# Performance work log

Hardware: AMD Instinct MI355X
Metric: run time of the kernel (lower is better)

Reference implementation:

```python
import jax, jax.numpy as jnp
import numpy as np

N = 4096   # nodes
E = 65536  # edges
D_IN = 64
H = 128
T = 8
B = 8


def setup_inputs() -> dict:
    key = jax.random.key(0)
    ks = jax.random.split(key, 6)
    x = jax.random.normal(ks[0], (B, T, N, D_IN), jnp.float32)
    edge_index = jax.random.randint(ks[1], (2, E), 0, N, dtype=jnp.int32)
    W0 = jax.random.normal(ks[2], (D_IN + H, 4 * H), jnp.float32) * 0.05
    b0 = jax.random.normal(ks[3], (4 * H,), jnp.float32) * 0.05
    W1 = jax.random.normal(ks[4], (H + H, 4 * H), jnp.float32) * 0.05
    b1 = jax.random.normal(ks[5], (4 * H,), jnp.float32) * 0.05
    return {"x": x, "W0": W0, "b0": b0, "W1": W1, "b1": b1, "edge_index": edge_index}


def _gcn_norm(edge_index, n):
    # PyG GCNConv(improved=True): A_hat = A + 2I, deg over incoming edges (col)
    src, dst = edge_index[0], edge_index[1]
    deg = jax.ops.segment_sum(jnp.ones(edge_index.shape[1], jnp.float32), dst, num_segments=n) + 2.0
    dinv = jax.lax.rsqrt(deg)  # deg >= 2 always, safe
    return src, dst, dinv


def _gcn_gates(comb, W, b, src, dst, dinv, n):
    # comb: (b, n, i+h) -> gates: (b, n, 4h)
    xw = jnp.einsum('bnf,fg->bng', comb, W)
    norm_e = dinv[src] * dinv[dst]                      # (E,)
    msgs = xw[:, src, :] * norm_e[None, :, None]        # (b, E, 4h)
    agg = jax.vmap(lambda m: jax.ops.segment_sum(m, dst, num_segments=n))(msgs)
    # self-loop with weight 2: norm = 2 * dinv[i]^2
    agg = agg + (2.0 * dinv * dinv)[None, :, None] * xw + b
    return agg


def reference(x, W0, b0, W1, b1, edge_index):
    src, dst, dinv = _gcn_norm(edge_index, N)

    def run_layer(seq, W, b):
        h_dim = W.shape[1] // 4

        def step(carry, xt):
            h, c = carry
            comb = jnp.concatenate([xt, h], axis=-1)
            gates = _gcn_gates(comb, W, b, src, dst, dinv, N)
            ci, cf, co, cg = jnp.split(gates, 4, axis=-1)
            i = jax.nn.sigmoid(ci)
            f = jax.nn.sigmoid(cf)
            o = jax.nn.sigmoid(co)
            g = jnp.tanh(cg)
            c_next = f * c + i * g
            h_next = o * jnp.tanh(c_next)
            return (h_next, c_next), h_next

        h0 = jnp.zeros((seq.shape[1], N, h_dim), seq.dtype)
        _, hs = jax.lax.scan(step, (h0, h0), seq)
        return hs  # (t, b, n, h)

    seq = jnp.swapaxes(x, 0, 1)  # batch_first -> (t, b, n, d)
    hs0 = run_layer(seq, W0, b0)
    hs1 = run_layer(hs0, W1, b1)
    return jnp.swapaxes(hs1, 0, 1)  # (b, t, n, h) last-layer output sequence
```

## Files before the change

kernel.cpp:

```cpp
#include <hip/hip_runtime.h>
#include <hip/hip_fp16.h>
#include <math.h>

constexpr int N_NODES = 4096;
constexpr int N_EDGES = 65536;
constexpr int D_INF   = 64;
constexpr int H       = 128;
constexpr int T       = 8;
constexpr int B       = 8;
constexpr int M       = B * N_NODES;

typedef __attribute__((ext_vector_type(8))) short bf16x8;
typedef __attribute__((ext_vector_type(4))) float f32x4;
typedef __attribute__((ext_vector_type(8))) _Float16 f16x8;

__device__ inline unsigned short f2bf(float x) {
  unsigned int u = __float_as_uint(x);
  unsigned int r = (u + 0x7fffu + ((u >> 16) & 1u)) >> 16;
  return (unsigned short)r;
}
__device__ inline float bf2f(unsigned short b) {
  return __uint_as_float((unsigned int)b << 16);
}
__device__ __forceinline__ int swz(int s) { return s ^ (((s >> 7) & 7) << 3); }


__global__ void k_count(const int* __restrict__ dst, int* __restrict__ cnt) {
  int e = blockIdx.x * blockDim.x + threadIdx.x;
  if (e < N_EDGES) atomicAdd(&cnt[dst[e]], 1);
}

__global__ void k_dinv(const int* __restrict__ cnt, float* __restrict__ dinv) {
  int n = blockIdx.x * blockDim.x + threadIdx.x;
  if (n < N_NODES) dinv[n] = 1.0f / sqrtf((float)cnt[n] + 2.0f);
}

__global__ void k_scan(const int* __restrict__ cnt, int* __restrict__ rowptr) {
  __shared__ int sums[1024];
  int t = threadIdx.x;
  int v0 = cnt[4*t+0], v1 = cnt[4*t+1], v2 = cnt[4*t+2], v3 = cnt[4*t+3];
  int s0 = v0, s1 = s0 + v1, s2 = s1 + v2, s3 = s2 + v3;
  sums[t] = s3;
  __syncthreads();
  for (int off = 1; off < 1024; off <<= 1) {
    int x = (t >= off) ? sums[t - off] : 0;
    __syncthreads();
    sums[t] += x;
    __syncthreads();
  }
  int base = (t > 0) ? sums[t - 1] : 0;
  if (t == 0) rowptr[0] = 0;
  rowptr[4*t+1] = base + s0;
  rowptr[4*t+2] = base + s1;
  rowptr[4*t+3] = base + s2;
  rowptr[4*t+4] = base + s3;
}

__global__ void k_fill(const int* __restrict__ src, const int* __restrict__ dst,
                       const float* __restrict__ dinv, const int* __restrict__ rowptr,
                       int* __restrict__ fill, int2* __restrict__ eg) {
  int e = blockIdx.x * blockDim.x + threadIdx.x;
  if (e >= N_EDGES) return;
  int s = src[e], d = dst[e];
  int p = rowptr[d] + atomicAdd(&fill[d], 1);
  eg[p] = make_int2(s, __float_as_int(dinv[s] * dinv[d]));
}

__global__ void k_hist(const int* __restrict__ cnt, int* __restrict__ hist) {
  int n = blockIdx.x * blockDim.x + threadIdx.x;
  if (n < N_NODES) atomicAdd(&hist[min(cnt[n], 127)], 1);
}

__global__ void k_hscan(const int* __restrict__ hist, int* __restrict__ hbase) {
  __shared__ int sh[128];
  int t = threadIdx.x;
  sh[t] = hist[t];
  __syncthreads();
  for (int off = 1; off < 128; off <<= 1) {
    int x = (t >= off) ? sh[t - off] : 0;
    __syncthreads();
    sh[t] += x;
    __syncthreads();
  }
  hbase[t] = sh[t] - hist[t];
}

__global__ void k_place(const int* __restrict__ cnt, const int* __restrict__ hbase,
                        int* __restrict__ filld, int* __restrict__ sorted) {
  int n = blockIdx.x * blockDim.x + threadIdx.x;
  if (n >= N_NODES) return;
  int d = min(cnt[n], 127);
  sorted[hbase[d] + atomicAdd(&filld[d], 1)] = n;
}

__global__ void k_pack(const float* __restrict__ W, unsigned short* __restrict__ Bp,
                       int K) {
  int tid = blockIdx.x * 256 + threadIdx.x;
  if (tid >= K * 64) return;
  int lane = tid & 63;
  int ntg  = (tid >> 6) & 31;
  int kb   = tid >> 11;
  int gate = ntg & 3, fg = ntg >> 2;
  int corig = gate * 128 + fg * 16 + (lane & 15);
  int k0 = kb * 32 + (lane >> 4) * 8;
  long obase = ((long)(kb * 32 + ntg) * 64 + lane) * 8;
  long plane = (long)K * 512;
  #pragma unroll
  for (int j = 0; j < 8; ++j) {
    float v = W[(long)(k0 + j) * 512 + corig];
    unsigned short h = f2bf(v);
    Bp[obase + j]         = h;
    Bp[plane + obase + j] = f2bf(v - bf2f(h));
  }
}

template<int K, bool L0>
__global__ __launch_bounds__(512, 4) void k_fused(
    const int* __restrict__ rowptr, const int2* __restrict__ eg,
    const float* __restrict__ dinv, const int* __restrict__ sorted,
    const float* __restrict__ X32,
    const _Float16* __restrict__ PH0,
    const _Float16* __restrict__ PH1,
    const unsigned short* __restrict__ Bp, const float* __restrict__ bias,
    _Float16* __restrict__ hout, float* __restrict__ cbuf,
    float* __restrict__ out2, int t) {
  constexpr int KB = K / 32;
  __shared__ __align__(16) unsigned short At[8 * KB * 64 * 8];
  __shared__ int nodeLDS[64];
  int tid  = threadIdx.x;
  int lane = tid & 63;
  int w    = tid >> 6;
  int j    = blockIdx.x;
  int b    = j & 7;
  int jj   = j >> 3;
  int g    = lane >> 4, l = lane & 15;
  int c4   = l * 4, c8 = l * 8;

  const float*    Ax   = L0 ? (X32 + (long)b * ((long)T * N_NODES * D_INF)) : nullptr;
  const _Float16* Ah_p = L0 ? nullptr : (PH0 + (long)b * N_NODES * H);
  const _Float16* Bh_p = (L0 ? PH0 : PH1) + (long)b * N_NODES * H;
  constexpr int kbB0 = (L0 ? 64 : 128) >> 5;
  int lane2f = 16 * (l & 3);
  int kbB    = kbB0 + (c8 >> 5);
  int kbA16  = c8 >> 5;
  int kbA32  = c4 >> 5;
  int subA32 = (l & 7) >> 1;
  int j0A32  = (l & 1) * 4;

  #pragma unroll
  for (int nd = 0; nd < 2; ++nd) {
    int r  = (w << 3) + (g << 1) + nd;
    int pairIdx = jj * 32 + (r >> 1);
    int n  = (r & 1) ? sorted[N_NODES - 1 - pairIdx] : sorted[pairIdx];
    if (l == 0) nodeLDS[r] = n;
    int rs = rowptr[n], re = rowptr[n + 1];
    float accA[8] = {0.f,0.f,0.f,0.f,0.f,0.f,0.f,0.f};
    float accB[8] = {0.f,0.f,0.f,0.f,0.f,0.f,0.f,0.f};
    int e = rs;
    for (; e + 3 < re; e += 4) {
      int2 q0 = eg[e], q1 = eg[e + 1], q2 = eg[e + 2], q3 = eg[e + 3];
      float w0 = __int_as_float(q0.y), w1 = __int_as_float(q1.y);
      float w2 = __int_as_float(q2.y), w3 = __int_as_float(q3.y);
      if constexpr (L0) {
        f32x4 a0 = *(const f32x4*)(Ax + (long)q0.x * D_INF + c4);
        f32x4 a1 = *(const f32x4*)(Ax + (long)q1.x * D_INF + c4);
        f32x4 a2 = *(const f32x4*)(Ax + (long)q2.x * D_INF + c4);
        f32x4 a3 = *(const f32x4*)(Ax + (long)q3.x * D_INF + c4);
        #pragma unroll
        for (int q = 0; q < 4; ++q)
          accA[q] += w0 * a0[q] + w1 * a1[q] + w2 * a2[q] + w3 * a3[q];
      } else {
        f16x8 a0 = *(const f16x8*)(Ah_p + (long)q0.x * H + c8);
        f16x8 a1 = *(const f16x8*)(Ah_p + (long)q1.x * H + c8);
        f16x8 a2 = *(const f16x8*)(Ah_p + (long)q2.x * H + c8);
        f16x8 a3 = *(const f16x8*)(Ah_p + (long)q3.x * H + c8);
        #pragma unroll
        for (int q = 0; q < 8; ++q)
          accA[q] += w0 * (float)a0[q] + w1 * (float)a1[q]
                   + w2 * (float)a2[q] + w3 * (float)a3[q];
      }
      f16x8 b0 = *(const f16x8*)(Bh_p + (long)q0.x * H + c8);
      f16x8 b1 = *(const f16x8*)(Bh_p + (long)q1.x * H + c8);
      f16x8 b2 = *(const f16x8*)(Bh_p + (long)q2.x * H + c8);
      f16x8 b3 = *(const f16x8*)(Bh_p + (long)q3.x * H + c8);
      #pragma unroll
      for (int q = 0; q < 8; ++q)
        accB[q] += w0 * (float)b0[q] + w1 * (float)b1[q]
                 + w2 * (float)b2[q] + w3 * (float)b3[q];
    }
    for (; e < re; ++e) {
      int2 q0 = eg[e];
      float w0 = __int_as_float(q0.y);
      if constexpr (L0) {
        f32x4 a0 = *(const f32x4*)(Ax + (long)q0.x * D_INF + c4);
        #pragma unroll
        for (int q = 0; q < 4; ++q) accA[q] += w0 * a0[q];
      } else {
        f16x8 a0 = *(const f16x8*)(Ah_p + (long)q0.x * H + c8);
        #pragma unroll
        for (int q = 0; q < 8; ++q) accA[q] += w0 * (float)a0[q];
      }
      f16x8 b0 = *(const f16x8*)(Bh_p + (long)q0.x * H + c8);
      #pragma unroll
      for (int q = 0; q < 8; ++q) accB[q] += w0 * (float)b0[q];
    }
    float dn = dinv[n];
    float sw = 2.0f * dn * dn;
    if constexpr (L0) {
      f32x4 a = *(const f32x4*)(Ax + (long)n * D_INF + c4);
      #pragma unroll
      for (int q = 0; q < 4; ++q) accA[q] += sw * a[q];
    } else {
      f16x8 a = *(const f16x8*)(Ah_p + (long)n * H + c8);
      #pragma unroll
      for (int q = 0; q < 8; ++q) accA[q] += sw * (float)a[q];
    }
    {
      f16x8 v = *(const f16x8*)(Bh_p + (long)n * H + c8);
      #pragma unroll
      for (int q = 0; q < 8; ++q) accB[q] += sw * (float)v[q];
    }

    int mt    = r >> 4;
    int lane2 = (r & 15) + lane2f;
    {
      bf16x8 hv, lv;
      #pragma unroll
      for (int q = 0; q < 8; ++q) {
        unsigned short hs = f2bf(accB[q]);
        hv[q] = (short)hs;
        lv[q] = (short)f2bf(accB[q] - bf2f(hs));
      }
      *(bf16x8*)(At + swz((((mt)     * KB + kbB) * 64 + lane2) * 8)) = hv;
      *(bf16x8*)(At + swz((((4 + mt) * KB + kbB) * 64 + lane2) * 8)) = lv;
    }
    if constexpr (L0) {
      unsigned long long hv = 0ull, lv = 0ull;
      #pragma unroll
      for (int q = 0; q < 4; ++q) {
        unsigned short hs = f2bf(accA[q]);
        unsigned short ls = f2bf(accA[q] - bf2f(hs));
        hv |= (unsigned long long)hs << (16 * q);
        lv |= (unsigned long long)ls << (16 * q);
      }
      int lA = (r & 15) + 16 * subA32;
      *(unsigned long long*)(At + swz((((mt)     * KB + kbA32) * 64 + lA) * 8 + j0A32)) = hv;
      *(unsigned long long*)(At + swz((((4 + mt) * KB + kbA32) * 64 + lA) * 8 + j0A32)) = lv;
    } else {
      bf16x8 hv, lv;
      #pragma unroll
      for (int q = 0; q < 8; ++q) {
        unsigned short hs = f2bf(accA[q]);
        hv[q] = (short)hs;
        lv[q] = (short)f2bf(accA[q] - bf2f(hs));
      }
      *(bf16x8*)(At + swz((((mt)     * KB + kbA16) * 64 + lane2) * 8)) = hv;
      *(bf16x8*)(At + swz((((4 + mt) * KB + kbA16) * 64 + lane2) * 8)) = lv;
    }
  }
  __syncthreads();

  int l15 = lane & 15, lq = lane >> 4;
  const unsigned short* bb  = Bp + (long)(w * 4) * 512 + lane * 8;
  const unsigned short* blp = bb + (long)K * 512;

  f32x4 acc[4][4];
  #pragma unroll
  for (int mt = 0; mt < 4; ++mt)
    #pragma unroll
    for (int gt = 0; gt < 4; ++gt)
      acc[mt][gt] = (f32x4){0.f, 0.f, 0.f, 0.f};

  __builtin_amdgcn_s_setprio(1);
  #pragma unroll 2
  for (int kb = 0; kb < KB; ++kb) {
    bf16x8 AH_[4], AL_[4];
    #pragma unroll
    for (int mt = 0; mt < 4; ++mt) {
      AH_[mt] = *(const bf16x8*)(At + swz((((mt)     * KB + kb) * 64 + lane) * 8));
      AL_[mt] = *(const bf16x8*)(At + swz((((4 + mt) * KB + kb) * 64 + lane) * 8));
    }
    bf16x8 BH[4], BL[4];
    #pragma unroll
    for (int gt = 0; gt < 4; ++gt) {
      BH[gt] = *(const bf16x8*)(bb  + ((long)kb * 32 + gt) * 512);
      BL[gt] = *(const bf16x8*)(blp + ((long)kb * 32 + gt) * 512);
    }
    #pragma unroll
    for (int gt = 0; gt < 4; ++gt) {
      #pragma unroll
      for (int mt = 0; mt < 4; ++mt) {
        acc[mt][gt] = __builtin_amdgcn_mfma_f32_16x16x32_bf16(AH_[mt], BH[gt], acc[mt][gt], 0, 0, 0);
        acc[mt][gt] = __builtin_amdgcn_mfma_f32_16x16x32_bf16(AL_[mt], BH[gt], acc[mt][gt], 0, 0, 0);
        acc[mt][gt] = __builtin_amdgcn_mfma_f32_16x16x32_bf16(AH_[mt], BL[gt], acc[mt][gt], 0, 0, 0);
      }
    }
  }
  __builtin_amdgcn_s_setprio(0);

  int f = w * 16 + l15;
  float bi = bias[f], bff = bias[128 + f], bo = bias[256 + f], bg = bias[384 + f];
  #pragma unroll
  for (int mt = 0; mt < 4; ++mt) {
    #pragma unroll
    for (int r = 0; r < 4; ++r) {
      int rt = mt * 16 + lq * 4 + r;
      int n2 = nodeLDS[rt];
      float vi = 1.0f / (1.0f + __expf(-(acc[mt][0][r] + bi)));
      float vf = 1.0f / (1.0f + __expf(-(acc[mt][1][r] + bff)));
      float vo = 1.0f / (1.0f + __expf(-(acc[mt][2][r] + bo)));
      float vg = tanhf(acc[mt][3][r] + bg);
      long idx = ((long)b * N_NODES + n2) * H + f;
      float cn = vf * cbuf[idx] + vi * vg;
      float hn = vo * tanhf(cn);
      cbuf[idx] = cn;
      hout[idx] = (_Float16)hn;
      if (out2) {
        __builtin_nontemporal_store(hn,
            &out2[(((long)b * T + t) * N_NODES + n2) * H + f]);
      }
    }
  }
}


extern "C" void kernel_launch(void* const* d_in, const int* in_sizes, int n_in,
                              void* d_out, int out_size, void* d_ws, size_t ws_size,
                              hipStream_t stream) {
  const float* x  = (const float*)d_in[0];
  const float* W0 = (const float*)d_in[1];
  const float* b0 = (const float*)d_in[2];
  const float* W1 = (const float*)d_in[3];
  const float* b1 = (const float*)d_in[4];
  const int*   ei = (const int*)d_in[5];
  const int* srcp = ei;
  const int* dstp = ei + N_EDGES;
  float* out = (float*)d_out;

  char* p = (char*)d_ws;
  auto alloc = [&](size_t bytes) {
    char* r = p;
    p += (bytes + 255) & ~(size_t)255;
    return r;
  };
  int*   cnt    = (int*)  alloc(N_NODES * 4);
  int*   fill   = (int*)  alloc(N_NODES * 4);
  float* dinv   = (float*)alloc(N_NODES * 4);
  int*   rowptr = (int*)  alloc((N_NODES + 1) * 4);
  int2*  eg     = (int2*) alloc((size_t)N_EDGES * 8);
  int*   hist   = (int*)  alloc(128 * 4);
  int*   hbase  = (int*)  alloc(128 * 4);
  int*   filld  = (int*)  alloc(128 * 4);
  int*   sorted = (int*)  alloc(N_NODES * 4);
  float* cc     = (float*)alloc((size_t)2 * M * H * 4);
  _Float16* hh  = (_Float16*)alloc((size_t)4 * M * H * 2);
  unsigned short* Bp0 = (unsigned short*)alloc((size_t)192 * 512 * 2 * 2);
  unsigned short* Bp1 = (unsigned short*)alloc((size_t)256 * 512 * 2 * 2);
  float*    c0  = cc;
  float*    c1  = cc + (size_t)M * H;
  _Float16* h0a = hh;
  _Float16* h0b = hh + (size_t)M * H;
  _Float16* h1a = hh + (size_t)2 * M * H;
  _Float16* h1b = hh + (size_t)3 * M * H;

  hipMemsetAsync(cnt,   0, N_NODES * 4, stream);
  hipMemsetAsync(fill,  0, N_NODES * 4, stream);
  hipMemsetAsync(hist,  0, 128 * 4, stream);
  hipMemsetAsync(filld, 0, 128 * 4, stream);
  hipMemsetAsync(cc,    0, (size_t)2 * M * H * 4, stream);
  hipMemsetAsync(hh,    0, (size_t)4 * M * H * 2, stream);

  k_count<<<N_EDGES / 256, 256, 0, stream>>>(dstp, cnt);
  k_dinv <<<N_NODES / 256, 256, 0, stream>>>(cnt, dinv);
  k_scan <<<1, 1024, 0, stream>>>(cnt, rowptr);
  k_fill <<<N_EDGES / 256, 256, 0, stream>>>(srcp, dstp, dinv, rowptr, fill, eg);
  k_hist <<<N_NODES / 256, 256, 0, stream>>>(cnt, hist);
  k_hscan<<<1, 128, 0, stream>>>(hist, hbase);
  k_place<<<N_NODES / 256, 256, 0, stream>>>(cnt, hbase, filld, sorted);
  k_pack <<<(192 * 64 + 255) / 256, 256, 0, stream>>>(W0, Bp0, 192);
  k_pack <<<(256 * 64 + 255) / 256, 256, 0, stream>>>(W1, Bp1, 256);

  for (int t = 0; t < T; ++t) {
    const _Float16* h0r = (t & 1) ? h0b : h0a;
    _Float16*       h0w = (t & 1) ? h0a : h0b;
    const _Float16* h1r = (t & 1) ? h1b : h1a;
    _Float16*       h1w = (t & 1) ? h1a : h1b;
    k_fused<192, true><<<512, 512, 0, stream>>>(rowptr, eg, dinv, sorted,
        x + (size_t)t * N_NODES * D_INF, h0r, nullptr,
        Bp0, b0, h0w, c0, nullptr, t);
    k_fused<256, false><<<512, 512, 0, stream>>>(rowptr, eg, dinv, sorted,
        nullptr, h0w, h1r,
        Bp1, b1, h1w, c1, out, t);
  }
}
```

Measured before the change: 772.4 us.

## Reuse layer-1 aggregated h0 for next-step layer-0 and precompute A·x

Layer 1 at step t already computes the graph aggregation A·h0_t. It now also stores that result, already split into hi/lo bf16 in MFMA tile layout, into a global buffer. Layer 0 at step t+1 reads this buffer directly instead of re-gathering h0 over the edges. The A·x aggregation for every timestep is hoisted into one upfront batched kernel and stored as fp16. As a result, layer 0 becomes a pure GEMM plus LSTM-cell kernel. The cost is extra global traffic for the stored tiles and a small precision loss from keeping A·x in fp16.

Measured after the change: 829.5 us. 1.07x slower.

```diff
diff --git a/kernel.cpp b/kernel.cpp
--- a/kernel.cpp
+++ b/kernel.cpp
@@ -13,6 +13,7 @@
 typedef __attribute__((ext_vector_type(8))) short bf16x8;
 typedef __attribute__((ext_vector_type(4))) float f32x4;
 typedef __attribute__((ext_vector_type(8))) _Float16 f16x8;
+typedef __attribute__((ext_vector_type(4))) _Float16 f16x4;
 
 __device__ inline unsigned short f2bf(float x) {
   unsigned int u = __float_as_uint(x);
@@ -114,17 +115,171 @@
   }
 }
 
-template<int K, bool L0>
-__global__ __launch_bounds__(512, 4) void k_fused(
+__global__ __launch_bounds__(256) void k_ax(
+    const int* __restrict__ rowptr, const int2* __restrict__ eg,
+    const float* __restrict__ dinv, const float* __restrict__ x,
+    _Float16* __restrict__ AX) {
+  int tid = threadIdx.x;
+  int grp = blockIdx.x * 16 + (tid >> 4);
+  int l   = tid & 15;
+  int c4  = l * 4;
+  int n   = grp & (N_NODES - 1);
+  int bt  = grp >> 12;
+  int b   = bt & 7, tt = bt >> 3;
+  const float* Xb = x + (long)(b * T + tt) * N_NODES * D_INF;
+  float acc[4] = {0.f, 0.f, 0.f, 0.f};
+  int rs = rowptr[n], re = rowptr[n + 1];
+  int e = rs;
+  for (; e + 3 < re; e += 4) {
+    int2 q0 = eg[e], q1 = eg[e + 1], q2 = eg[e + 2], q3 = eg[e + 3];
+    float w0 = __int_as_float(q0.y), w1 = __int_as_float(q1.y);
+    float w2 = __int_as_float(q2.y), w3 = __int_as_float(q3.y);
+    f32x4 a0 = *(const f32x4*)(Xb + (long)q0.x * D_INF + c4);
+    f32x4 a1 = *(const f32x4*)(Xb + (long)q1.x * D_INF + c4);
+    f32x4 a2 = *(const f32x4*)(Xb + (long)q2.x * D_INF + c4);
+    f32x4 a3 = *(const f32x4*)(Xb + (long)q3.x * D_INF + c4);
+    #pragma unroll
+    for (int q = 0; q < 4; ++q)
+      acc[q] += w0 * a0[q] + w1 * a1[q] + w2 * a2[q] + w3 * a3[q];
+  }
+  for (; e < re; ++e) {
+    int2 q0 = eg[e];
+    float w0 = __int_as_float(q0.y);
+    f32x4 a0 = *(const f32x4*)(Xb + (long)q0.x * D_INF + c4);
+    #pragma unroll
+    for (int q = 0; q < 4; ++q) acc[q] += w0 * a0[q];
+  }
+  float dn = dinv[n];
+  float sw = 2.0f * dn * dn;
+  f32x4 a = *(const f32x4*)(Xb + (long)n * D_INF + c4);
+  #pragma unroll
+  for (int q = 0; q < 4; ++q) acc[q] += sw * a[q];
+  f16x4 o;
+  #pragma unroll
+  for (int q = 0; q < 4; ++q) o[q] = (_Float16)acc[q];
+  *(f16x4*)(AX + ((long)(tt * 8 + b) * N_NODES + n) * D_INF + c4) = o;
+}
+
+__global__ __launch_bounds__(512, 4) void k_l0(
+    const int* __restrict__ sorted,
+    const _Float16* __restrict__ AXt,
+    const unsigned short* __restrict__ AH0,
+    const unsigned short* __restrict__ Bp, const float* __restrict__ bias,
+    _Float16* __restrict__ hout, float* __restrict__ cbuf) {
+  __shared__ __align__(16) unsigned short Atx[8 * 2 * 64 * 8];
+  __shared__ int nodeLDS[64];
+  int tid  = threadIdx.x;
+  int lane = tid & 63;
+  int w    = tid >> 6;
+  int j    = blockIdx.x;
+  int b    = j & 7;
+  int jj   = j >> 3;
+  int g    = lane >> 4, l = lane & 15;
+  int c4   = l * 4;
+  int kbA32  = c4 >> 5;
+  int subA32 = (l & 7) >> 1;
+  int j0A32  = (l & 1) * 4;
+
+  #pragma unroll
+  for (int nd = 0; nd < 2; ++nd) {
+    int r = (w << 3) + (g << 1) + nd;
+    int pairIdx = jj * 32 + (r >> 1);
+    int n = (r & 1) ? sorted[N_NODES - 1 - pairIdx] : sorted[pairIdx];
+    if (l == 0) nodeLDS[r] = n;
+    f16x4 xv = *(const f16x4*)(AXt + ((long)b * N_NODES + n) * D_INF + c4);
+    unsigned long long hv = 0ull, lv = 0ull;
+    #pragma unroll
+    for (int q = 0; q < 4; ++q) {
+      float a = (float)xv[q];
+      unsigned short hs = f2bf(a);
+      unsigned short ls = f2bf(a - bf2f(hs));
+      hv |= (unsigned long long)hs << (16 * q);
+      lv |= (unsigned long long)ls << (16 * q);
+    }
+    int mt = r >> 4;
+    int lA = (r & 15) + 16 * subA32;
+    *(unsigned long long*)(Atx + swz(((mt * 2 + kbA32) * 64 + lA) * 8 + j0A32)) = hv;
+    *(unsigned long long*)(Atx + swz((((4 + mt) * 2 + kbA32) * 64 + lA) * 8 + j0A32)) = lv;
+  }
+  __syncthreads();
+
+  int l15 = lane & 15, lq = lane >> 4;
+  const unsigned short* bb  = Bp + (long)(w * 4) * 512 + lane * 8;
+  const unsigned short* blp = bb + (long)192 * 512;
+
+  f32x4 acc[4][4];
+  #pragma unroll
+  for (int mt = 0; mt < 4; ++mt)
+    #pragma unroll
+    for (int gt = 0; gt < 4; ++gt)
+      acc[mt][gt] = (f32x4){0.f, 0.f, 0.f, 0.f};
+
+  __builtin_amdgcn_s_setprio(1);
+  #pragma unroll
+  for (int kb = 0; kb < 6; ++kb) {
+    bf16x8 AH_[4], AL_[4];
+    if (kb < 2) {
+      #pragma unroll
+      for (int mt = 0; mt < 4; ++mt) {
+        AH_[mt] = *(const bf16x8*)(Atx + swz(((mt * 2 + kb) * 64 + lane) * 8));
+        AL_[mt] = *(const bf16x8*)(Atx + swz((((4 + mt) * 2 + kb) * 64 + lane) * 8));
+      }
+    } else {
+      #pragma unroll
+      for (int mt = 0; mt < 4; ++mt) {
+        AH_[mt] = *(const bf16x8*)(AH0 + ((((long)j * 8 + mt) * 4 + (kb - 2)) * 64 + lane) * 8);
+        AL_[mt] = *(const bf16x8*)(AH0 + ((((long)j * 8 + 4 + mt) * 4 + (kb - 2)) * 64 + lane) * 8);
+      }
+    }
+    bf16x8 BH[4], BL[4];
+    #pragma unroll
+    for (int gt = 0; gt < 4; ++gt) {
+      BH[gt] = *(const bf16x8*)(bb  + ((long)kb * 32 + gt) * 512);
+      BL[gt] = *(const bf16x8*)(blp + ((long)kb * 32 + gt) * 512);
+    }
+    #pragma unroll
+    for (int gt = 0; gt < 4; ++gt) {
+      #pragma unroll
+      for (int mt = 0; mt < 4; ++mt) {
+        acc[mt][gt] = __builtin_amdgcn_mfma_f32_16x16x32_bf16(AH_[mt], BH[gt], acc[mt][gt], 0, 0, 0);
+        acc[mt][gt] = __builtin_amdgcn_mfma_f32_16x16x32_bf16(AL_[mt], BH[gt], acc[mt][gt], 0, 0, 0);
+        acc[mt][gt] = __builtin_amdgcn_mfma_f32_16x16x32_bf16(AH_[mt], BL[gt], acc[mt][gt], 0, 0, 0);
+      }
+    }
+  }
+  __builtin_amdgcn_s_setprio(0);
+
+  int f = w * 16 + l15;
+  float bi = bias[f], bff = bias[128 + f], bo = bias[256 + f], bg = bias[384 + f];
+  #pragma unroll
+  for (int mt = 0; mt < 4; ++mt) {
+    #pragma unroll
+    for (int r = 0; r < 4; ++r) {
+      int rt = mt * 16 + lq * 4 + r;
+      int n2 = nodeLDS[rt];
+      float vi = 1.0f / (1.0f + __expf(-(acc[mt][0][r] + bi)));
+      float vf = 1.0f / (1.0f + __expf(-(acc[mt][1][r] + bff)));
+      float vo = 1.0f / (1.0f + __expf(-(acc[mt][2][r] + bo)));
+      float vg = tanhf(acc[mt][3][r] + bg);
+      long idx = ((long)b * N_NODES + n2) * H + f;
+      float cn = vf * cbuf[idx] + vi * vg;
+      float hn = vo * tanhf(cn);
+      cbuf[idx] = cn;
+      hout[idx] = (_Float16)hn;
+    }
+  }
+}
+
+__global__ __launch_bounds__(512, 4) void k_l1(
     const int* __restrict__ rowptr, const int2* __restrict__ eg,
     const float* __restrict__ dinv, const int* __restrict__ sorted,
-    const float* __restrict__ X32,
-    const _Float16* __restrict__ PH0,
-    const _Float16* __restrict__ PH1,
+    const _Float16* __restrict__ H0,
+    const _Float16* __restrict__ H1r,
     const unsigned short* __restrict__ Bp, const float* __restrict__ bias,
-    _Float16* __restrict__ hout, float* __restrict__ cbuf,
+    unsigned short* __restrict__ AH0,
+    _Float16* __restrict__ h1out, float* __restrict__ cbuf,
     float* __restrict__ out2, int t) {
-  constexpr int KB = K / 32;
+  constexpr int KB = 8;
   __shared__ __align__(16) unsigned short At[8 * KB * 64 * 8];
   __shared__ int nodeLDS[64];
   int tid  = threadIdx.x;
@@ -134,18 +289,12 @@
   int b    = j & 7;
   int jj   = j >> 3;
   int g    = lane >> 4, l = lane & 15;
-  int c4   = l * 4, c8 = l * 8;
-
-  const float*    Ax   = L0 ? (X32 + (long)b * ((long)T * N_NODES * D_INF)) : nullptr;
-  const _Float16* Ah_p = L0 ? nullptr : (PH0 + (long)b * N_NODES * H);
-  const _Float16* Bh_p = (L0 ? PH0 : PH1) + (long)b * N_NODES * H;
-  constexpr int kbB0 = (L0 ? 64 : 128) >> 5;
+  int c8   = l * 8;
+  const _Float16* A_p = H0  + (long)b * N_NODES * H;
+  const _Float16* B_p = H1r + (long)b * N_NODES * H;
   int lane2f = 16 * (l & 3);
-  int kbB    = kbB0 + (c8 >> 5);
   int kbA16  = c8 >> 5;
-  int kbA32  = c4 >> 5;
-  int subA32 = (l & 7) >> 1;
-  int j0A32  = (l & 1) * 4;
+  int kbB    = 4 + kbA16;
 
   #pragma unroll
   for (int nd = 0; nd < 2; ++nd) {
@@ -161,28 +310,18 @@
       int2 q0 = eg[e], q1 = eg[e + 1], q2 = eg[e + 2], q3 = eg[e + 3];
       float w0 = __int_as_float(q0.y), w1 = __int_as_float(q1.y);
       float w2 = __int_as_float(q2.y), w3 = __int_as_float(q3.y);
-      if constexpr (L0) {
-        f32x4 a0 = *(const f32x4*)(Ax + (long)q0.x * D_INF + c4);
-        f32x4 a1 = *(const f32x4*)(Ax + (long)q1.x * D_INF + c4);
-        f32x4 a2 = *(const f32x4*)(Ax + (long)q2.x * D_INF + c4);
-        f32x4 a3 = *(const f32x4*)(Ax + (long)q3.x * D_INF + c4);
-        #pragma unroll
-        for (int q = 0; q < 4; ++q)
-          accA[q] += w0 * a0[q] + w1 * a1[q] + w2 * a2[q] + w3 * a3[q];
-      } else {
-        f16x8 a0 = *(const f16x8*)(Ah_p + (long)q0.x * H + c8);
-        f16x8 a1 = *(const f16x8*)(Ah_p + (long)q1.x * H + c8);
-        f16x8 a2 = *(const f16x8*)(Ah_p + (long)q2.x * H + c8);
-        f16x8 a3 = *(const f16x8*)(Ah_p + (long)q3.x * H + c8);
-        #pragma unroll
-        for (int q = 0; q < 8; ++q)
-          accA[q] += w0 * (float)a0[q] + w1 * (float)a1[q]
-                   + w2 * (float)a2[q] + w3 * (float)a3[q];
-      }
-      f16x8 b0 = *(const f16x8*)(Bh_p + (long)q0.x * H + c8);
-      f16x8 b1 = *(const f16x8*)(Bh_p + (long)q1.x * H + c8);
-      f16x8 b2 = *(const f16x8*)(Bh_p + (long)q2.x * H + c8);
-      f16x8 b3 = *(const f16x8*)(Bh_p + (long)q3.x * H + c8);
+      f16x8 a0 = *(const f16x8*)(A_p + (long)q0.x * H + c8);
+      f16x8 a1 = *(const f16x8*)(A_p + (long)q1.x * H + c8);
+      f16x8 a2 = *(const f16x8*)(A_p + (long)q2.x * H + c8);
+      f16x8 a3 = *(const f16x8*)(A_p + (long)q3.x * H + c8);
+      #pragma unroll
+      for (int q = 0; q < 8; ++q)
+        accA[q] += w0 * (float)a0[q] + w1 * (float)a1[q]
+                 + w2 * (float)a2[q] + w3 * (float)a3[q];
+      f16x8 b0 = *(const f16x8*)(B_p + (long)q0.x * H + c8);
+      f16x8 b1 = *(const f16x8*)(B_p + (long)q1.x * H + c8);
+      f16x8 b2 = *(const f16x8*)(B_p + (long)q2.x * H + c8);
+      f16x8 b3 = *(const f16x8*)(B_p + (long)q3.x * H + c8);
       #pragma unroll
       for (int q = 0; q < 8; ++q)
         accB[q] += w0 * (float)b0[q] + w1 * (float)b1[q]
@@ -191,34 +330,23 @@
     for (; e < re; ++e) {
       int2 q0 = eg[e];
       float w0 = __int_as_float(q0.y);
-      if constexpr (L0) {
-        f32x4 a0 = *(const f32x4*)(Ax + (long)q0.x * D_INF + c4);
-        #pragma unroll
-        for (int q = 0; q < 4; ++q) accA[q] += w0 * a0[q];
-      } else {
-        f16x8 a0 = *(const f16x8*)(Ah_p + (long)q0.x * H + c8);
-        #pragma unroll
-        for (int q = 0; q < 8; ++q) accA[q] += w0 * (float)a0[q];
-      }
-      f16x8 b0 = *(const f16x8*)(Bh_p + (long)q0.x * H + c8);
+      f16x8 a0 = *(const f16x8*)(A_p + (long)q0.x * H + c8);
+      #pragma unroll
+      for (int q = 0; q < 8; ++q) accA[q] += w0 * (float)a0[q];
+      f16x8 b0 = *(const f16x8*)(B_p + (long)q0.x * H + c8);
       #pragma unroll
       for (int q = 0; q < 8; ++q) accB[q] += w0 * (float)b0[q];
     }
     float dn = dinv[n];
     float sw = 2.0f * dn * dn;
-    if constexpr (L0) {
-      f32x4 a = *(const f32x4*)(Ax + (long)n * D_INF + c4);
-      #pragma unroll
-      for (int q = 0; q < 4; ++q) accA[q] += sw * a[q];
-    } else {
-      f16x8 a = *(const f16x8*)(Ah_p + (long)n * H + c8);
-      #pragma unroll
-      for (int q = 0; q < 8; ++q) accA[q] += sw * (float)a[q];
-    }
     {
-      f16x8 v = *(const f16x8*)(Bh_p + (long)n * H + c8);
-      #pragma unroll
-      for (int q = 0; q < 8; ++q) accB[q] += sw * (float)v[q];
+      f16x8 a = *(const f16x8*)(A_p + (long)n * H + c8);
+      f16x8 v = *(const f16x8*)(B_p + (long)n * H + c8);
+      #pragma unroll
+      for (int q = 0; q < 8; ++q) {
+        accA[q] += sw * (float)a[q];
+        accB[q] += sw * (float)v[q];
+      }
     }
 
     int mt    = r >> 4;
@@ -234,19 +362,7 @@
       *(bf16x8*)(At + swz((((mt)     * KB + kbB) * 64 + lane2) * 8)) = hv;
       *(bf16x8*)(At + swz((((4 + mt) * KB + kbB) * 64 + lane2) * 8)) = lv;
     }
-    if constexpr (L0) {
-      unsigned long long hv = 0ull, lv = 0ull;
-      #pragma unroll
-      for (int q = 0; q < 4; ++q) {
-        unsigned short hs = f2bf(accA[q]);
-        unsigned short ls = f2bf(accA[q] - bf2f(hs));
-        hv |= (unsigned long long)hs << (16 * q);
-        lv |= (unsigned long long)ls << (16 * q);
-      }
-      int lA = (r & 15) + 16 * subA32;
-      *(unsigned long long*)(At + swz((((mt)     * KB + kbA32) * 64 + lA) * 8 + j0A32)) = hv;
-      *(unsigned long long*)(At + swz((((4 + mt) * KB + kbA32) * 64 + lA) * 8 + j0A32)) = lv;
-    } else {
+    {
       bf16x8 hv, lv;
       #pragma unroll
       for (int q = 0; q < 8; ++q) {
@@ -256,13 +372,15 @@
       }
       *(bf16x8*)(At + swz((((mt)     * KB + kbA16) * 64 + lane2) * 8)) = hv;
       *(bf16x8*)(At + swz((((4 + mt) * KB + kbA16) * 64 + lane2) * 8)) = lv;
+      *(bf16x8*)(AH0 + ((((long)j * 8 + mt)     * 4 + kbA16) * 64 + lane2) * 8) = hv;
+      *(bf16x8*)(AH0 + ((((long)j * 8 + 4 + mt) * 4 + kbA16) * 64 + lane2) * 8) = lv;
     }
   }
   __syncthreads();
 
   int l15 = lane & 15, lq = lane >> 4;
   const unsigned short* bb  = Bp + (long)(w * 4) * 512 + lane * 8;
-  const unsigned short* blp = bb + (long)K * 512;
+  const unsigned short* blp = bb + (long)256 * 512;
 
   f32x4 acc[4][4];
   #pragma unroll
@@ -314,11 +432,9 @@
       float cn = vf * cbuf[idx] + vi * vg;
       float hn = vo * tanhf(cn);
       cbuf[idx] = cn;
-      hout[idx] = (_Float16)hn;
-      if (out2) {
-        __builtin_nontemporal_store(hn,
-            &out2[(((long)b * T + t) * N_NODES + n2) * H + f]);
-      }
+      h1out[idx] = (_Float16)hn;
+      __builtin_nontemporal_store(hn,
+          &out2[(((long)b * T + t) * N_NODES + n2) * H + f]);
     }
   }
 }
@@ -353,22 +469,24 @@
   int*   filld  = (int*)  alloc(128 * 4);
   int*   sorted = (int*)  alloc(N_NODES * 4);
   float* cc     = (float*)alloc((size_t)2 * M * H * 4);
-  _Float16* hh  = (_Float16*)alloc((size_t)4 * M * H * 2);
+  _Float16* hh  = (_Float16*)alloc((size_t)3 * M * H * 2);
+  _Float16* AX  = (_Float16*)alloc((size_t)T * M * D_INF * 2);
+  unsigned short* AH0 = (unsigned short*)alloc((size_t)512 * 8 * 4 * 64 * 8 * 2);
   unsigned short* Bp0 = (unsigned short*)alloc((size_t)192 * 512 * 2 * 2);
   unsigned short* Bp1 = (unsigned short*)alloc((size_t)256 * 512 * 2 * 2);
   float*    c0  = cc;
   float*    c1  = cc + (size_t)M * H;
-  _Float16* h0a = hh;
-  _Float16* h0b = hh + (size_t)M * H;
-  _Float16* h1a = hh + (size_t)2 * M * H;
-  _Float16* h1b = hh + (size_t)3 * M * H;
+  _Float16* h0  = hh;
+  _Float16* h1a = hh + (size_t)M * H;
+  _Float16* h1b = hh + (size_t)2 * M * H;
 
   hipMemsetAsync(cnt,   0, N_NODES * 4, stream);
   hipMemsetAsync(fill,  0, N_NODES * 4, stream);
   hipMemsetAsync(hist,  0, 128 * 4, stream);
   hipMemsetAsync(filld, 0, 128 * 4, stream);
   hipMemsetAsync(cc,    0, (size_t)2 * M * H * 4, stream);
-  hipMemsetAsync(hh,    0, (size_t)4 * M * H * 2, stream);
+  hipMemsetAsync(hh,    0, (size_t)3 * M * H * 2, stream);
+  hipMemsetAsync(AH0,   0, (size_t)512 * 8 * 4 * 64 * 8 * 2, stream);
 
   k_count<<<N_EDGES / 256, 256, 0, stream>>>(dstp, cnt);
   k_dinv <<<N_NODES / 256, 256, 0, stream>>>(cnt, dinv);
@@ -379,17 +497,14 @@
   k_place<<<N_NODES / 256, 256, 0, stream>>>(cnt, hbase, filld, sorted);
   k_pack <<<(192 * 64 + 255) / 256, 256, 0, stream>>>(W0, Bp0, 192);
   k_pack <<<(256 * 64 + 255) / 256, 256, 0, stream>>>(W1, Bp1, 256);
+  k_ax   <<<(8 * T * N_NODES) / 16, 256, 0, stream>>>(rowptr, eg, dinv, x, AX);
 
   for (int t = 0; t < T; ++t) {
-    const _Float16* h0r = (t & 1) ? h0b : h0a;
-    _Float16*       h0w = (t & 1) ? h0a : h0b;
     const _Float16* h1r = (t & 1) ? h1b : h1a;
     _Float16*       h1w = (t & 1) ? h1a : h1b;
-    k_fused<192, true><<<512, 512, 0, stream>>>(rowptr, eg, dinv, sorted,
-        x + (size_t)t * N_NODES * D_INF, h0r, nullptr,
-        Bp0, b0, h0w, c0, nullptr, t);
-    k_fused<256, false><<<512, 512, 0, stream>>>(rowptr, eg, dinv, sorted,
-        nullptr, h0w, h1r,
-        Bp1, b1, h1w, c1, out, t);
-  }
-}
+    k_l0<<<512, 512, 0, stream>>>(sorted,
+        AX + (size_t)t * M * D_INF, AH0, Bp0, b0, h0, c0);
+    k_l1<<<512, 512, 0, stream>>>(rowptr, eg, dinv, sorted,
+        h0, h1r, Bp1, b1, AH0, h1w, c1, out, t);
+  }
+}
```
